# Optimization experiments

Hardware: AMD Instinct MI355X
Metric: run time of the kernel (lower is better)

## Reference

```python
import jax, jax.numpy as jnp
import numpy as np

BATCH, MAXPV = 32, 50
RULENUM, PROPNUM = 256, 256  # must be equal (eye(rulenum) * property_importance)
ENT_DIM, RULE_DIM = 128, 128
ENTITYNUM = 50000
THRESHOLD = 0.5


def _l2norm(x, eps=1e-12):
    # F.normalize(p=2, dim=-1)
    n = jnp.linalg.norm(x, axis=-1, keepdims=True)
    return x / jnp.clip(n, eps)


def setup_inputs() -> dict:
    key = jax.random.key(0)
    ks = jax.random.split(key, 20)
    d_in = ENT_DIM + RULE_DIM
    inp = {
        'property': jax.random.randint(ks[0], (BATCH, MAXPV), 0, ENTITYNUM),
        'value': jax.random.randint(ks[1], (BATCH, MAXPV), 0, ENTITYNUM),
        'samemask': jax.random.randint(ks[2], (BATCH, MAXPV), 0, 2),
        'padmask': jax.random.randint(ks[3], (BATCH, MAXPV), 0, 2),
        'rule_embedding': jax.random.normal(ks[4], (RULENUM, RULE_DIM), jnp.float32),
        'entity_table': jax.random.normal(ks[5], (ENTITYNUM, ENT_DIM), jnp.float32),
        # Linear weights stored (in, out); concat order in the original is (p_emb, rule_emb)
        'fc1_w': jax.random.normal(ks[6], (d_in, ENT_DIM), jnp.float32),
        'fc1_b': jax.random.normal(ks[7], (ENT_DIM,), jnp.float32) * 0.02,
        'fc2_w': jax.random.normal(ks[8], (d_in, ENT_DIM), jnp.float32),
        'fc2_b': jax.random.normal(ks[9], (ENT_DIM,), jnp.float32) * 0.02,
        'fc3_w': jax.random.normal(ks[10], (d_in, ENT_DIM), jnp.float32),
        'fc3_b': jax.random.normal(ks[11], (ENT_DIM,), jnp.float32) * 0.02,
        'fc4_w': jax.random.normal(ks[12], (ENT_DIM, 1), jnp.float32) * 0.05,
        'fc4_b': jax.random.normal(ks[13], (1,), jnp.float32) * 0.02,
        'fc5_w': jax.random.normal(ks[14], (ENT_DIM, 1), jnp.float32) * 0.05,
        'fc5_b': jax.random.normal(ks[15], (1,), jnp.float32) * 0.02,
        'fc6_w': jax.random.normal(ks[16], (ENT_DIM, ENT_DIM), jnp.float32) * 0.05,
        'fc6_b': jax.random.normal(ks[17], (ENT_DIM,), jnp.float32) * 0.02,
    }
    return inp


def reference(property, value, samemask, padmask, rule_embedding, entity_table,
              fc1_w, fc1_b, fc2_w, fc2_b, fc3_w, fc3_b,
              fc4_w, fc4_b, fc5_w, fc5_b, fc6_w, fc6_b):
    E = entity_table.shape[1]
    R = rule_embedding.shape[0]
    P = R  # propertynum == rulenum (required by eye() regularizer)

    p_emb = _l2norm(entity_table[property])   # (B, M, E)
    v_emb = _l2norm(entity_table[value])      # (B, M, E)
    r_emb = _l2norm(rule_embedding)           # (R, Dr)

    # cat(p, rule) -> Linear decomposed into two smaller matmuls (same math)
    def branch(w, b):
        return p_emb @ w[:E], r_emb @ w[E:] + b  # (B,M,Eo), (R,Eo)

    # s1 branch
    pa, ra = branch(fc1_w, fc1_b)
    h1 = jax.nn.relu(pa[:, None, :, :] + ra[None, :, None, :])   # (B,R,M,E)
    s1 = jax.nn.sigmoid(h1 @ fc4_w + fc4_b)[..., 0]              # (B,R,M)

    # p branch
    pb, rb = branch(fc2_w, fc2_b)
    h2 = jax.nn.relu(pb[:, None, :, :] + rb[None, :, None, :])
    p = jax.nn.sigmoid(h2 @ fc5_w + fc5_b)[..., 0]               # (B,R,M)

    # s2 branch
    pc, rc = branch(fc3_w, fc3_b)
    h3 = jax.nn.relu(pc[:, None, :, :] + rc[None, :, None, :])
    gv = _l2norm(h3 @ fc6_w + fc6_b)                             # (B,R,M,E)
    vb = v_emb[:, None, :, :]                                    # (B,1,M,E)
    denom = jnp.clip(jnp.linalg.norm(vb, axis=-1) * jnp.linalg.norm(gv, axis=-1), 1e-8)
    cos = jnp.sum(vb * gv, axis=-1) / denom
    s2 = 0.5 * cos + 0.5                                         # (B,R,M)

    score = p + (1.0 - p) * s2
    score = jnp.where(samemask[:, None, :] == 1, s1 * score, 1.0 - s1)

    # property importance K: fc1/fc4 on cat(prop_emb, rule_emb)
    prop_emb = _l2norm(entity_table[:P])                         # propertyids = arange(P)
    pi_h = jax.nn.relu((prop_emb @ fc1_w[:E])[None, :, :]
                       + (r_emb @ fc1_w[E:] + fc1_b)[:, None, :])  # (R,P,E)
    pi = jax.nn.sigmoid(pi_h @ fc4_w + fc4_b)[..., 0]            # (R,P)

    rule_mask = jnp.sum(pi * (pi > THRESHOLD), axis=-1) + 1.0    # (R,)

    score = score * padmask[:, None, :].astype(score.dtype)
    score = score * (s1 > THRESHOLD)
    score = jnp.sum(score, axis=-1) / rule_mask[None, :]          # (B,R)
    pooledscore = jnp.max(score, axis=1)                          # (B,)

    diag = jnp.eye(R, dtype=pi.dtype)
    reg = pi * diag + (1.0 - pi) * (1.0 - diag)
    reg = -jnp.log(reg + 1e-8) * (1.0 - diag + diag * R)
    reg_logits = jnp.mean(reg)
    return pooledscore, reg_logits
```

## Files before the change

kernel.cpp:

```cpp
#include <hip/hip_runtime.h>
#include <hip/hip_bf16.h>

#define BATCH 32
#define MAXPV 50
#define RN 256
#define PN 256
#define DIM 128
#define NI (BATCH*MAXPV)

typedef unsigned short u16;
typedef __attribute__((ext_vector_type(8))) short short8;
typedef __attribute__((ext_vector_type(4))) float f32x4;

__device__ float g_pa[NI*DIM], g_pb[NI*DIM], g_pc[NI*DIM];
__device__ float g_pp1[PN*DIM];
__device__ __attribute__((aligned(16))) float g_ra[RN*DIM];
__device__ __attribute__((aligned(16))) float g_rb[RN*DIM];
__device__ float g_rmask[RN], g_regp[RN];
__device__ float g_scores[(size_t)NI*RN];
__device__ short8 g_bfrag[8][4][64];
__device__ __attribute__((aligned(16))) float g_rcA[16*4*64*8];

#define WS_WLS(ws)  ((int2*)((ws)+4))
#define WS_WLD(ws)  ((ws)+4+3200)

__device__ __forceinline__ float bf2f(u16 u){ return __uint_as_float(((unsigned)u)<<16); }
__device__ __forceinline__ float LD(const void* p, size_t i, bool bf){
    return bf ? bf2f(((const u16*)p)[i]) : ((const float*)p)[i];
}
__device__ __forceinline__ int LDI(const void* p, size_t i, bool w64){
    return w64 ? (int)((const long long*)p)[i] : ((const int*)p)[i];
}
__device__ __forceinline__ short f2bf(float f){
    unsigned u = __float_as_uint(f);
    u = (u + 0x7FFFu + ((u>>16)&1u)) >> 16;
    return (short)u;
}
__device__ __forceinline__ unsigned f2bf2(float x, float y){
    float2 f; f.x=x; f.y=y;
    __hip_bfloat162 h = __float22bfloat162_rn(f);
    union { __hip_bfloat162 h; unsigned u; } c; c.h=h; return c.u;
}
__device__ __forceinline__ bool det_bf16(const void* ent){
    int l = threadIdx.x & 63;
    u16 v = ((const u16*)ent)[(size_t)2*(l*4)*977];
    int e = (v>>7)&0xFF;
    return __popcll(__ballot(e>=120 && e<=133)) >= 48;
}
__device__ __forceinline__ bool det_i64(const void* prop){
    int l = threadIdx.x & 63;
    bool z = (l<32) ? (((const unsigned*)prop)[2*l+1]==0u) : false;
    return __popcll(__ballot(z)) >= 30;
}
__device__ __forceinline__ float wred(float v){
#pragma unroll
    for(int o=32;o;o>>=1) v += __shfl_xor(v,o,64);
    return v;
}
__device__ __forceinline__ double wredd(double v){
#pragma unroll
    for(int o=32;o;o>>=1) v += __shfl_xor(v,o,64);
    return v;
}
__device__ __forceinline__ float wmax(float v){
#pragma unroll
    for(int o=32;o;o>>=1) v = fmaxf(v,__shfl_xor(v,o,64));
    return v;
}

__global__ __launch_bounds__(256) void k_pre(
    const void* __restrict__ ent, const void* __restrict__ rule,
    const void* __restrict__ prop, const void* __restrict__ val,
    const void* __restrict__ same, const void* __restrict__ pad,
    const void* __restrict__ fc6w,
    const void* __restrict__ fc1w, const void* __restrict__ fc2w, const void* __restrict__ fc3w,
    const void* __restrict__ fc1b, const void* __restrict__ fc2b, const void* __restrict__ fc3b,
    int* __restrict__ ws){
    const bool bf = det_bf16(ent);
    const int blk = blockIdx.x, tid = threadIdx.x;
    if(blk >= 372){
        const bool w64 = det_i64(prop);
        int i = (blk-372)*256 + tid;
        if(i < NI){
            int pd = LDI(pad,i,w64);
            if(pd==1){
                int sm = LDI(same,i,w64);
                if(sm==1){
                    int x = atomicAdd(ws+0,1);
                    WS_WLS(ws)[x] = make_int2(i, LDI(val,i,w64));
                } else {
                    int x = atomicAdd(ws+1,1);
                    WS_WLD(ws)[x] = i;
                }
            }
        }
        return;
    }
    if(blk >= 364){
        int nt = blk-364;
        int ks = tid>>6, lane = tid&63;
        int n = nt*16 + (lane&15);
        int k0 = ks*32 + (lane>>4)*8;
        short8 v;
#pragma unroll
        for(int j=0;j<8;j++) v[j] = f2bf(LD(fc6w,(size_t)(k0+j)*DIM + n, bf));
        g_bfrag[nt][ks][lane] = v;
        if(nt==0){
            g_rmask[tid] = 1.f; g_regp[tid] = 0.f;
            const bool w64 = det_i64(prop);
            if(tid==0) ws[2] = (bf?1:0) | (w64?2:0);
        }
        return;
    }
    __shared__ float s_w[64*DIM];
    __shared__ float s_in[16*DIM];
    __shared__ float s_bias[DIM];
    const void* w; size_t woff=0; const void* bptr=nullptr;
    float* out=nullptr; int row0; int mode=0; int srcsel;
    if(blk < 300){
        int wsel = blk/100; row0 = (blk%100)*16; srcsel = 0;
        w   = (wsel==0)?fc1w:(wsel==1)?fc2w:fc3w;
        out = (wsel==0)?g_pa:(wsel==1)?g_pb:g_pc;
    } else if(blk < 348){
        int rblk = blk-300; int wsel = rblk>>4; row0 = (rblk&15)*16; srcsel = 1;
        w    = (wsel==0)?fc1w:(wsel==1)?fc2w:fc3w;
        bptr = (wsel==0)?fc1b:(wsel==1)?fc2b:fc3b;
        woff = DIM*DIM; mode = wsel+1;
    } else { row0=(blk-348)*16; w=fc1w; out=g_pp1; srcsel=2; }
    const bool w64 = (srcsel==0) ? det_i64(prop) : false;
    {
        const int l = tid & 63;
        for(int it=0; it<4; it++){
            int lr = it*4 + (tid>>6);
            int row = row0 + lr;
            const void* src; size_t off;
            if(srcsel==0){ src=ent;  off=(size_t)LDI(prop,row,w64)*DIM; }
            else if(srcsel==1){ src=rule; off=(size_t)row*DIM; }
            else { src=ent; off=(size_t)row*DIM; }
            float a = LD(src,off+l,bf), b = LD(src,off+l+64,bf);
            float n = fmaxf(sqrtf((float)wredd((double)a*a+(double)b*b)), 1e-12f);
            s_in[lr*DIM+l]=a/n; s_in[lr*DIM+l+64]=b/n;
        }
    }
    if(tid<DIM) s_bias[tid] = bptr ? LD(bptr,tid,bf) : 0.f;
    const int j = tid & 127;
    const int rb8 = (tid>>7)*8;
    double acc[8] = {0,0,0,0,0,0,0,0};
    for(int half=0; half<2; half++){
        __syncthreads();
        for(int t=tid; t<64*DIM; t+=256)
            s_w[t] = LD(w, woff + (size_t)(half*64 + (t>>7))*DIM + (t&127), bf);
        __syncthreads();
        for(int k=0;k<64;k++){
            float wk = s_w[k*DIM + j];
#pragma unroll
            for(int rr=0;rr<8;rr++)
                acc[rr] += (double)s_in[(rb8+rr)*DIM + half*64 + k]*(double)wk;
        }
    }
    const double bj = (double)s_bias[j];
#pragma unroll
    for(int rr=0;rr<8;rr++){
        const int row = row0 + rb8 + rr;
        const float vv = (float)(bj + acc[rr]);
        if(mode==0)      out[(size_t)row*DIM + j] = vv;
        else if(mode==1) g_ra[(size_t)row*DIM + j] = vv;
        else if(mode==2) g_rb[(size_t)row*DIM + j] = vv;
        else {
            int mt=row>>4, am=row&15, ks=j>>5, quad=(j>>3)&3, jj=j&7;
            g_rcA[((mt*4+ks)*64 + quad*16+am)*8 + jj] = vv;
        }
    }
}

__global__ __launch_bounds__(256) void k_score(
    const void* __restrict__ ent,
    const void* __restrict__ fc4w, const void* __restrict__ fc4b,
    const void* __restrict__ fc5w, const void* __restrict__ fc5b,
    const void* __restrict__ fc6b, const int* __restrict__ ws){
    const int blk = blockIdx.x, tid = threadIdx.x;
    const int fl = ws[2];
    const bool bf = fl & 1;
    if(blk < 64){
        __shared__ float s_a[4][DIM];
        __shared__ double s_pf4[DIM];
        const int i0 = blk*4;
        if(tid<DIM) s_pf4[tid]=(double)LD(fc4w,tid,bf);
        for(int t=tid; t<4*DIM; t+=256){
            int ii=t>>7, k=t&127;
            s_a[ii][k] = g_pp1[(size_t)(i0+ii)*DIM+k];
        }
        __syncthreads();
        const int r = tid;
        const float4* rap = (const float4*)&g_ra[(size_t)r*DIM];
        double d0=0.0, d1=0.0, d2=0.0, d3=0.0;
#pragma unroll 4
        for(int x=0; x<32; x++){
            const float4 ra = rap[x];
#pragma unroll
            for(int cc=0; cc<4; cc++){
                const int k = x*4 + cc;
                const float rav = (cc==0)?ra.x:(cc==1)?ra.y:(cc==2)?ra.z:ra.w;
                const double f4k = s_pf4[k];
                d0 += (double)fmaxf(s_a[0][k]+rav,0.f)*f4k;
                d1 += (double)fmaxf(s_a[1][k]+rav,0.f)*f4k;
                d2 += (double)fmaxf(s_a[2][k]+rav,0.f)*f4k;
                d3 += (double)fmaxf(s_a[3][k]+rav,0.f)*f4k;
            }
        }
        const double b4 = (double)LD(fc4b,0,bf);
        double d[4] = {d0,d1,d2,d3};
        float mask_sum = 0.f, reg_sum = 0.f;
#pragma unroll
        for(int ii=0;ii<4;ii++){
            int p = i0 + ii;
            double sd = d[ii] + b4;
            float piv = 1.f/(1.f+expf(-(float)sd));
            if(sd > 0.0) mask_sum += piv;
            float eff = (p==r) ? piv : (1.f - piv);
            float wgt = (p==r) ? (float)RN : 1.f;
            reg_sum += -logf(eff + 1e-8f)*wgt;
        }
        atomicAdd(&g_rmask[r], mask_sum);
        atomicAdd(&g_regp[r], reg_sum);
        return;
    }
    int w2 = blk - 64;
    const int ns4 = ws[0]*4;

    __shared__ float s_pa[DIM], s_pb[DIM], s_pc[DIM], s_v[DIM], s_f5[DIM];
    __shared__ double s_f4[DIM];
    __shared__ float s_s1[64], s_p[64];
    __shared__ float s_st[64][4][2];

    if(w2 >= ns4){
        w2 -= ns4;
        if(w2 >= ws[1]) return;
        const int i = WS_WLD(ws)[w2];
        if(tid < 128){
            s_pa[tid] = g_pa[(size_t)i*DIM + tid];
            s_f4[tid] = (double)LD(fc4w,tid,bf);
        }
        __syncthreads();
        const int r = tid;
        const float4* rap = (const float4*)&g_ra[(size_t)r*DIM];
        double d = 0.0;
#pragma unroll 4
        for(int x=0; x<32; x++){
            const float4 ra = rap[x];
            d += (double)fmaxf(s_pa[x*4+0]+ra.x,0.f)*s_f4[x*4+0];
            d += (double)fmaxf(s_pa[x*4+1]+ra.y,0.f)*s_f4[x*4+1];
            d += (double)fmaxf(s_pa[x*4+2]+ra.z,0.f)*s_f4[x*4+2];
            d += (double)fmaxf(s_pa[x*4+3]+ra.w,0.f)*s_f4[x*4+3];
        }
        const double b4 = (double)LD(fc4b,0,bf);
        double sd = d + b4;
        float s1v = 1.f/(1.f+expf(-(float)sd));
        g_scores[(size_t)i*RN + r] = (sd > 0.0) ? (1.f - s1v) : 0.f;
        return;
    }

    const int2 e = WS_WLS(ws)[w2>>2];
    const int i = e.x, vi = e.y, q4 = w2 & 3;

    if(tid < DIM){
        s_pa[tid] = g_pa[(size_t)i*DIM + tid];
        s_pb[tid] = g_pb[(size_t)i*DIM + tid];
        s_pc[tid] = g_pc[(size_t)i*DIM + tid];
        s_f4[tid] = (double)LD(fc4w,tid,bf);
        s_f5[tid] = LD(fc5w,tid,bf);
    } else if(tid < 192){
        const int l = tid - 128;
        size_t off = (size_t)vi*DIM;
        float a = LD(ent,off+l,bf), b = LD(ent,off+l+64,bf);
        float n = fmaxf(sqrtf((float)wredd((double)a*a+(double)b*b)), 1e-12f);
        s_v[l]=a/n; s_v[l+64]=b/n;
    }
    __syncthreads();

    const int rr = tid & 63;
    const int r = q4*64 + rr;
    if(tid < 64){
        const float4* rap = (const float4*)&g_ra[(size_t)r*DIM];
        double d = 0.0;
#pragma unroll 4
        for(int x=0; x<32; x++){
            const float4 ra = rap[x];
            d += (double)fmaxf(s_pa[x*4+0]+ra.x,0.f)*s_f4[x*4+0];
            d += (double)fmaxf(s_pa[x*4+1]+ra.y,0.f)*s_f4[x*4+1];
            d += (double)fmaxf(s_pa[x*4+2]+ra.z,0.f)*s_f4[x*4+2];
            d += (double)fmaxf(s_pa[x*4+3]+ra.w,0.f)*s_f4[x*4+3];
        }
        const double b4 = (double)LD(fc4b,0,bf);
        double sd = d + b4;
        float s1v = 1.f/(1.f+expf(-(float)sd));
        s_s1[rr] = (sd > 0.0) ? s1v : -s1v;
    } else if(tid < 128){
        const float4* rbp = (const float4*)&g_rb[(size_t)r*DIM];
        float pq = 0.f;
#pragma unroll 4
        for(int x=0; x<32; x++){
            const float4 rb = rbp[x];
            pq = fmaf(fmaxf(s_pb[x*4+0]+rb.x,0.f), s_f5[x*4+0], pq);
            pq = fmaf(fmaxf(s_pb[x*4+1]+rb.y,0.f), s_f5[x*4+1], pq);
            pq = fmaf(fmaxf(s_pb[x*4+2]+rb.z,0.f), s_f5[x*4+2], pq);
            pq = fmaf(fmaxf(s_pb[x*4+3]+rb.w,0.f), s_f5[x*4+3], pq);
        }
        const float b5 = LD(fc5b,0,bf);
        s_p[rr] = 1.f/(1.f+expf(-(pq + b5)));
    }
    __syncthreads();

    const int w = tid>>6, l = tid&63;
    const int am = l&15, quad = l>>4;
    short8 bA[4], bB[4];
#pragma unroll
    for(int ks=0; ks<4; ks++){ bA[ks]=g_bfrag[2*w][ks][l]; bB[ks]=g_bfrag[2*w+1][ks][l]; }
    const int n0 = w*32 + am, n1 = n0 + 16;
    const float v0 = s_v[n0], v1 = s_v[n1];
    const float b60 = LD(fc6b, n0, bf), b61 = LD(fc6b, n1, bf);
    float vl = s_v[l], vh = s_v[l+64];
    const float nvb = sqrtf(wred(vl*vl + vh*vh));

    int mt = q4*4;
    float4 c[8];
#pragma unroll
    for(int ks=0; ks<4; ks++){
        const float* rp = &g_rcA[((mt*4+ks)*64 + l)*8];
        c[2*ks]   = *(const float4*)rp;
        c[2*ks+1] = *(const float4*)(rp+4);
    }
    for(int mtl=0; mtl<4; mtl++){
        float4 n[8];
        if(mtl < 3){
#pragma unroll
            for(int ks=0; ks<4; ks++){
                const float* rp = &g_rcA[(((mt+1)*4+ks)*64 + l)*8];
                n[2*ks]   = *(const float4*)rp;
                n[2*ks+1] = *(const float4*)(rp+4);
            }
        }
        short8 a[4];
#pragma unroll
        for(int ks=0; ks<4; ks++){
            const float4 p0 = *(const float4*)&s_pc[ks*32 + quad*8];
            const float4 p1 = *(const float4*)&s_pc[ks*32 + quad*8 + 4];
            const float4 c0 = c[2*ks], c1 = c[2*ks+1];
            union { short8 s; unsigned u[4]; } t;
            t.u[0] = f2bf2(fmaxf(p0.x+c0.x,0.f), fmaxf(p0.y+c0.y,0.f));
            t.u[1] = f2bf2(fmaxf(p0.z+c0.z,0.f), fmaxf(p0.w+c0.w,0.f));
            t.u[2] = f2bf2(fmaxf(p1.x+c1.x,0.f), fmaxf(p1.y+c1.y,0.f));
            t.u[3] = f2bf2(fmaxf(p1.z+c1.z,0.f), fmaxf(p1.w+c1.w,0.f));
            a[ks] = t.s;
        }
        f32x4 acc0 = {0.f,0.f,0.f,0.f}, acc1 = {0.f,0.f,0.f,0.f};
#pragma unroll
        for(int ks=0; ks<4; ks++){
            acc0 = __builtin_amdgcn_mfma_f32_16x16x32_bf16(a[ks], bA[ks], acc0, 0,0,0);
            acc1 = __builtin_amdgcn_mfma_f32_16x16x32_bf16(a[ks], bB[ks], acc1, 0,0,0);
        }
#pragma unroll
        for(int q=0; q<4; q++){
            float x0 = acc0[q] + b60;
            float x1 = acc1[q] + b61;
            float ss = x0*x0 + x1*x1;
            float dv = x0*v0 + x1*v1;
#pragma unroll
            for(int o=1;o<16;o<<=1){ ss += __shfl_xor(ss,o,64); dv += __shfl_xor(dv,o,64); }
            if(am==0){
                int row = mtl*16 + quad*4 + q;
                s_st[row][w][0] = ss;
                s_st[row][w][1] = dv;
            }
        }
#pragma unroll
        for(int x=0;x<8;x++) c[x] = n[x];
        mt++;
    }
    __syncthreads();
    if(tid < 64){
        const int r2 = q4*64 + tid;
        float ss = s_st[tid][0][0]+s_st[tid][1][0]+s_st[tid][2][0]+s_st[tid][3][0];
        float dv = s_st[tid][0][1]+s_st[tid][1][1]+s_st[tid][2][1]+s_st[tid][3][1];
        float s1 = fabsf(s_s1[tid]);
        float gate = (s_s1[tid] > 0.f) ? 1.f : 0.f;
        float pp = s_p[tid];
        float nx = sqrtf(ss);
        float clipnx = fmaxf(nx, 1e-12f);
        float gvn = nx/clipnx;
        float denom = fmaxf(nvb*gvn, 1e-8f);
        float cosv = (dv/clipnx)/denom;
        float s2 = 0.5f*cosv + 0.5f;
        float sc = s1*(pp + (1.f-pp)*s2);
        g_scores[(size_t)i*RN + r2] = sc * gate;
    }
}

__global__ void k_fin(float* __restrict__ out, const void* __restrict__ pad,
                      const int* __restrict__ ws){
    const bool w64 = (ws[2] & 2) != 0;
    const int blk = blockIdx.x, tid = threadIdx.x;
    const int w = tid>>6, l = tid&63;
    __shared__ float s[4];
    if(blk < 32){
        __shared__ int s_pad[MAXPV];
        if(tid < MAXPV) s_pad[tid] = LDI(pad, (size_t)blk*MAXPV + tid, w64);
        __syncthreads();
        float ssum = 0.f;
        for(int pv=0; pv<MAXPV; pv++){
            if(!s_pad[pv]) continue;
            ssum += g_scores[((size_t)blk*MAXPV + pv)*RN + tid];
        }
        float sc = ssum / g_rmask[tid];
        float m = wmax(sc);
        if(l==0) s[w]=m;
        __syncthreads();
        if(tid==0) out[blk] = fmaxf(fmaxf(s[0],s[1]), fmaxf(s[2],s[3]));
    } else {
        float v = g_regp[tid];
        v = wred(v);
        if(l==0) s[w]=v;
        __syncthreads();
        if(tid==0) out[32] = (s[0]+s[1]+s[2]+s[3]) / (float)(RN*PN);
    }
}

extern "C" void kernel_launch(void* const* d_in, const int* in_sizes, int n_in,
                              void* d_out, int out_size, void* d_ws, size_t ws_size,
                              hipStream_t stream){
    int map[18]; for(int i=0;i<18;i++) map[i]=i;
    if(n_in>=18 && in_sizes[0]==6400000){
        const int a[18] = {14,17,16,13,15,0,2,1,4,3,6,5,8,7,10,9,12,11};
        for(int i=0;i<18;i++) map[i]=a[i];
    }
    const void* prop = d_in[map[0]];
    const void* val  = d_in[map[1]];
    const void* same = d_in[map[2]];
    const void* pad  = d_in[map[3]];
    const void* rule = d_in[map[4]];
    const void* ent  = d_in[map[5]];
    const void* fc1w = d_in[map[6]];
    const void* fc1b = d_in[map[7]];
    const void* fc2w = d_in[map[8]];
    const void* fc2b = d_in[map[9]];
    const void* fc3w = d_in[map[10]];
    const void* fc3b = d_in[map[11]];
    const void* fc4w = d_in[map[12]];
    const void* fc4b = d_in[map[13]];
    const void* fc5w = d_in[map[14]];
    const void* fc5b = d_in[map[15]];
    const void* fc6w = d_in[map[16]];
    const void* fc6b = d_in[map[17]];

    hipMemsetAsync(d_ws, 0, 16, stream);
    k_pre<<<379, 256, 0, stream>>>(ent, rule, prop, val, same, pad, fc6w,
                                   fc1w, fc2w, fc3w, fc1b, fc2b, fc3b, (int*)d_ws);
    k_score<<<64 + 4*NI, 256, 0, stream>>>(ent, fc4w, fc4b, fc5w, fc5b, fc6b,
                                           (const int*)d_ws);
    k_fin<<<33, 256, 0, stream>>>((float*)d_out, pad, (const int*)d_ws);
}
```

Baseline: 192.2 us.

## Convert score kernel to persistent work-stealing loop and precompute value norms

The score kernel becomes a persistent kernel launched with a fixed 1536 blocks. Each block takes its first item from its block index, then pulls further work items from an atomic counter, so no blocks are launched only to exit early. The per-item L2 normalisation of value embeddings moves into extra k_pre blocks that write g_v, and the same-list now stores only the item index. This trades the cost of launching 6464 mostly empty blocks for an extra global buffer, atomic traffic and a barrier per work item, and it drops the software prefetch of rcA tiles.

After: 202.0 us. +5.1%, slower.

```diff
diff --git a/kernel.cpp b/kernel.cpp
--- a/kernel.cpp
+++ b/kernel.cpp
@@ -14,6 +14,7 @@
 
 __device__ float g_pa[NI*DIM], g_pb[NI*DIM], g_pc[NI*DIM];
 __device__ float g_pp1[PN*DIM];
+__device__ __attribute__((aligned(16))) float g_v[NI*DIM];
 __device__ __attribute__((aligned(16))) float g_ra[RN*DIM];
 __device__ __attribute__((aligned(16))) float g_rb[RN*DIM];
 __device__ float g_rmask[RN], g_regp[RN];
@@ -21,8 +22,8 @@
 __device__ short8 g_bfrag[8][4][64];
 __device__ __attribute__((aligned(16))) float g_rcA[16*4*64*8];
 
-#define WS_WLS(ws)  ((int2*)((ws)+4))
-#define WS_WLD(ws)  ((ws)+4+3200)
+#define WS_WLS(ws)  ((ws)+4)
+#define WS_WLD(ws)  ((ws)+4+1600)
 
 __device__ __forceinline__ float bf2f(u16 u){ return __uint_as_float(((unsigned)u)<<16); }
 __device__ __forceinline__ float LD(const void* p, size_t i, bool bf){
@@ -78,6 +79,16 @@
     int* __restrict__ ws){
     const bool bf = det_bf16(ent);
     const int blk = blockIdx.x, tid = threadIdx.x;
+    if(blk >= 379){
+        const bool w64 = det_i64(prop);
+        const int row = (blk-379)*4 + (tid>>6);
+        const int l = tid & 63;
+        size_t off = (size_t)LDI(val,row,w64)*DIM;
+        float a = LD(ent,off+l,bf), b = LD(ent,off+l+64,bf);
+        float n = fmaxf(sqrtf((float)wredd((double)a*a+(double)b*b)), 1e-12f);
+        g_v[(size_t)row*DIM+l]=a/n; g_v[(size_t)row*DIM+l+64]=b/n;
+        return;
+    }
     if(blk >= 372){
         const bool w64 = det_i64(prop);
         int i = (blk-372)*256 + tid;
@@ -87,7 +98,7 @@
                 int sm = LDI(same,i,w64);
                 if(sm==1){
                     int x = atomicAdd(ws+0,1);
-                    WS_WLS(ws)[x] = make_int2(i, LDI(val,i,w64));
+                    WS_WLS(ws)[x] = i;
                 } else {
                     int x = atomicAdd(ws+1,1);
                     WS_WLD(ws)[x] = i;
@@ -173,226 +184,212 @@
     }
 }
 
-__global__ __launch_bounds__(256) void k_score(
-    const void* __restrict__ ent,
+__global__ __launch_bounds__(256) void k_main(
     const void* __restrict__ fc4w, const void* __restrict__ fc4b,
     const void* __restrict__ fc5w, const void* __restrict__ fc5b,
-    const void* __restrict__ fc6b, const int* __restrict__ ws){
-    const int blk = blockIdx.x, tid = threadIdx.x;
-    const int fl = ws[2];
-    const bool bf = fl & 1;
-    if(blk < 64){
-        __shared__ float s_a[4][DIM];
-        __shared__ double s_pf4[DIM];
-        const int i0 = blk*4;
-        if(tid<DIM) s_pf4[tid]=(double)LD(fc4w,tid,bf);
-        for(int t=tid; t<4*DIM; t+=256){
-            int ii=t>>7, k=t&127;
-            s_a[ii][k] = g_pp1[(size_t)(i0+ii)*DIM+k];
-        }
-        __syncthreads();
-        const int r = tid;
-        const float4* rap = (const float4*)&g_ra[(size_t)r*DIM];
-        double d0=0.0, d1=0.0, d2=0.0, d3=0.0;
-#pragma unroll 4
-        for(int x=0; x<32; x++){
-            const float4 ra = rap[x];
-#pragma unroll
-            for(int cc=0; cc<4; cc++){
-                const int k = x*4 + cc;
-                const float rav = (cc==0)?ra.x:(cc==1)?ra.y:(cc==2)?ra.z:ra.w;
-                const double f4k = s_pf4[k];
-                d0 += (double)fmaxf(s_a[0][k]+rav,0.f)*f4k;
-                d1 += (double)fmaxf(s_a[1][k]+rav,0.f)*f4k;
-                d2 += (double)fmaxf(s_a[2][k]+rav,0.f)*f4k;
-                d3 += (double)fmaxf(s_a[3][k]+rav,0.f)*f4k;
-            }
-        }
-        const double b4 = (double)LD(fc4b,0,bf);
-        double d[4] = {d0,d1,d2,d3};
-        float mask_sum = 0.f, reg_sum = 0.f;
-#pragma unroll
-        for(int ii=0;ii<4;ii++){
-            int p = i0 + ii;
-            double sd = d[ii] + b4;
-            float piv = 1.f/(1.f+expf(-(float)sd));
-            if(sd > 0.0) mask_sum += piv;
-            float eff = (p==r) ? piv : (1.f - piv);
-            float wgt = (p==r) ? (float)RN : 1.f;
-            reg_sum += -logf(eff + 1e-8f)*wgt;
-        }
-        atomicAdd(&g_rmask[r], mask_sum);
-        atomicAdd(&g_regp[r], reg_sum);
-        return;
-    }
-    int w2 = blk - 64;
-    const int ns4 = ws[0]*4;
-
+    const void* __restrict__ fc6b, int* __restrict__ ws){
+    __shared__ int s_hdr[4];
     __shared__ float s_pa[DIM], s_pb[DIM], s_pc[DIM], s_v[DIM], s_f5[DIM];
     __shared__ double s_f4[DIM];
     __shared__ float s_s1[64], s_p[64];
     __shared__ float s_st[64][4][2];
-
-    if(w2 >= ns4){
-        w2 -= ns4;
-        if(w2 >= ws[1]) return;
-        const int i = WS_WLD(ws)[w2];
-        if(tid < 128){
-            s_pa[tid] = g_pa[(size_t)i*DIM + tid];
-            s_f4[tid] = (double)LD(fc4w,tid,bf);
-        }
-        __syncthreads();
-        const int r = tid;
-        const float4* rap = (const float4*)&g_ra[(size_t)r*DIM];
-        double d = 0.0;
-#pragma unroll 4
-        for(int x=0; x<32; x++){
-            const float4 ra = rap[x];
-            d += (double)fmaxf(s_pa[x*4+0]+ra.x,0.f)*s_f4[x*4+0];
-            d += (double)fmaxf(s_pa[x*4+1]+ra.y,0.f)*s_f4[x*4+1];
-            d += (double)fmaxf(s_pa[x*4+2]+ra.z,0.f)*s_f4[x*4+2];
-            d += (double)fmaxf(s_pa[x*4+3]+ra.w,0.f)*s_f4[x*4+3];
-        }
-        const double b4 = (double)LD(fc4b,0,bf);
-        double sd = d + b4;
-        float s1v = 1.f/(1.f+expf(-(float)sd));
-        g_scores[(size_t)i*RN + r] = (sd > 0.0) ? (1.f - s1v) : 0.f;
-        return;
-    }
-
-    const int2 e = WS_WLS(ws)[w2>>2];
-    const int i = e.x, vi = e.y, q4 = w2 & 3;
-
-    if(tid < DIM){
-        s_pa[tid] = g_pa[(size_t)i*DIM + tid];
-        s_pb[tid] = g_pb[(size_t)i*DIM + tid];
-        s_pc[tid] = g_pc[(size_t)i*DIM + tid];
-        s_f4[tid] = (double)LD(fc4w,tid,bf);
-        s_f5[tid] = LD(fc5w,tid,bf);
-    } else if(tid < 192){
-        const int l = tid - 128;
-        size_t off = (size_t)vi*DIM;
-        float a = LD(ent,off+l,bf), b = LD(ent,off+l+64,bf);
-        float n = fmaxf(sqrtf((float)wredd((double)a*a+(double)b*b)), 1e-12f);
-        s_v[l]=a/n; s_v[l+64]=b/n;
-    }
+    __shared__ float s_a[4][DIM];
+    const int tid = threadIdx.x;
+    if(tid==0){ int4 h = *(const int4*)ws; s_hdr[0]=h.x; s_hdr[1]=h.y; s_hdr[2]=h.z; }
     __syncthreads();
-
-    const int rr = tid & 63;
-    const int r = q4*64 + rr;
-    if(tid < 64){
-        const float4* rap = (const float4*)&g_ra[(size_t)r*DIM];
-        double d = 0.0;
-#pragma unroll 4
-        for(int x=0; x<32; x++){
-            const float4 ra = rap[x];
-            d += (double)fmaxf(s_pa[x*4+0]+ra.x,0.f)*s_f4[x*4+0];
-            d += (double)fmaxf(s_pa[x*4+1]+ra.y,0.f)*s_f4[x*4+1];
-            d += (double)fmaxf(s_pa[x*4+2]+ra.z,0.f)*s_f4[x*4+2];
-            d += (double)fmaxf(s_pa[x*4+3]+ra.w,0.f)*s_f4[x*4+3];
-        }
-        const double b4 = (double)LD(fc4b,0,bf);
-        double sd = d + b4;
-        float s1v = 1.f/(1.f+expf(-(float)sd));
-        s_s1[rr] = (sd > 0.0) ? s1v : -s1v;
-    } else if(tid < 128){
-        const float4* rbp = (const float4*)&g_rb[(size_t)r*DIM];
-        float pq = 0.f;
-#pragma unroll 4
-        for(int x=0; x<32; x++){
-            const float4 rb = rbp[x];
-            pq = fmaf(fmaxf(s_pb[x*4+0]+rb.x,0.f), s_f5[x*4+0], pq);
-            pq = fmaf(fmaxf(s_pb[x*4+1]+rb.y,0.f), s_f5[x*4+1], pq);
-            pq = fmaf(fmaxf(s_pb[x*4+2]+rb.z,0.f), s_f5[x*4+2], pq);
-            pq = fmaf(fmaxf(s_pb[x*4+3]+rb.w,0.f), s_f5[x*4+3], pq);
-        }
-        const float b5 = LD(fc5b,0,bf);
-        s_p[rr] = 1.f/(1.f+expf(-(pq + b5)));
-    }
-    __syncthreads();
-
-    const int w = tid>>6, l = tid&63;
-    const int am = l&15, quad = l>>4;
+    const int nsame = s_hdr[0], ndiff = s_hdr[1];
+    const bool bf = s_hdr[2] & 1;
+    const int total = 64 + 4*nsame + ndiff;
+    if(tid < DIM){ s_f4[tid] = (double)LD(fc4w,tid,bf); s_f5[tid] = LD(fc5w,tid,bf); }
+    const int w = tid>>6, l = tid&63, am = l&15, quad = l>>4;
     short8 bA[4], bB[4];
 #pragma unroll
     for(int ks=0; ks<4; ks++){ bA[ks]=g_bfrag[2*w][ks][l]; bB[ks]=g_bfrag[2*w+1][ks][l]; }
     const int n0 = w*32 + am, n1 = n0 + 16;
-    const float v0 = s_v[n0], v1 = s_v[n1];
     const float b60 = LD(fc6b, n0, bf), b61 = LD(fc6b, n1, bf);
-    float vl = s_v[l], vh = s_v[l+64];
-    const float nvb = sqrtf(wred(vl*vl + vh*vh));
-
-    int mt = q4*4;
-    float4 c[8];
-#pragma unroll
-    for(int ks=0; ks<4; ks++){
-        const float* rp = &g_rcA[((mt*4+ks)*64 + l)*8];
-        c[2*ks]   = *(const float4*)rp;
-        c[2*ks+1] = *(const float4*)(rp+4);
-    }
-    for(int mtl=0; mtl<4; mtl++){
-        float4 n[8];
-        if(mtl < 3){
-#pragma unroll
-            for(int ks=0; ks<4; ks++){
-                const float* rp = &g_rcA[(((mt+1)*4+ks)*64 + l)*8];
-                n[2*ks]   = *(const float4*)rp;
-                n[2*ks+1] = *(const float4*)(rp+4);
-            }
-        }
-        short8 a[4];
-#pragma unroll
-        for(int ks=0; ks<4; ks++){
-            const float4 p0 = *(const float4*)&s_pc[ks*32 + quad*8];
-            const float4 p1 = *(const float4*)&s_pc[ks*32 + quad*8 + 4];
-            const float4 c0 = c[2*ks], c1 = c[2*ks+1];
-            union { short8 s; unsigned u[4]; } t;
-            t.u[0] = f2bf2(fmaxf(p0.x+c0.x,0.f), fmaxf(p0.y+c0.y,0.f));
-            t.u[1] = f2bf2(fmaxf(p0.z+c0.z,0.f), fmaxf(p0.w+c0.w,0.f));
-            t.u[2] = f2bf2(fmaxf(p1.x+c1.x,0.f), fmaxf(p1.y+c1.y,0.f));
-            t.u[3] = f2bf2(fmaxf(p1.z+c1.z,0.f), fmaxf(p1.w+c1.w,0.f));
-            a[ks] = t.s;
-        }
-        f32x4 acc0 = {0.f,0.f,0.f,0.f}, acc1 = {0.f,0.f,0.f,0.f};
-#pragma unroll
-        for(int ks=0; ks<4; ks++){
-            acc0 = __builtin_amdgcn_mfma_f32_16x16x32_bf16(a[ks], bA[ks], acc0, 0,0,0);
-            acc1 = __builtin_amdgcn_mfma_f32_16x16x32_bf16(a[ks], bB[ks], acc1, 0,0,0);
-        }
-#pragma unroll
-        for(int q=0; q<4; q++){
-            float x0 = acc0[q] + b60;
-            float x1 = acc1[q] + b61;
-            float ss = x0*x0 + x1*x1;
-            float dv = x0*v0 + x1*v1;
-#pragma unroll
-            for(int o=1;o<16;o<<=1){ ss += __shfl_xor(ss,o,64); dv += __shfl_xor(dv,o,64); }
-            if(am==0){
-                int row = mtl*16 + quad*4 + q;
-                s_st[row][w][0] = ss;
-                s_st[row][w][1] = dv;
-            }
-        }
-#pragma unroll
-        for(int x=0;x<8;x++) c[x] = n[x];
-        mt++;
-    }
-    __syncthreads();
-    if(tid < 64){
-        const int r2 = q4*64 + tid;
-        float ss = s_st[tid][0][0]+s_st[tid][1][0]+s_st[tid][2][0]+s_st[tid][3][0];
-        float dv = s_st[tid][0][1]+s_st[tid][1][1]+s_st[tid][2][1]+s_st[tid][3][1];
-        float s1 = fabsf(s_s1[tid]);
-        float gate = (s_s1[tid] > 0.f) ? 1.f : 0.f;
-        float pp = s_p[tid];
-        float nx = sqrtf(ss);
-        float clipnx = fmaxf(nx, 1e-12f);
-        float gvn = nx/clipnx;
-        float denom = fmaxf(nvb*gvn, 1e-8f);
-        float cosv = (dv/clipnx)/denom;
-        float s2 = 0.5f*cosv + 0.5f;
-        float sc = s1*(pp + (1.f-pp)*s2);
-        g_scores[(size_t)i*RN + r2] = sc * gate;
+    const double b4 = (double)LD(fc4b,0,bf);
+    const float b5 = LD(fc5b,0,bf);
+
+    for(int it=0;; it++){
+        int idx;
+        if(it==0) idx = blockIdx.x;
+        else {
+            if(tid==0) s_hdr[3] = atomicAdd(ws+3, 1);
+            __syncthreads();
+            idx = (int)gridDim.x + s_hdr[3];
+        }
+        if(idx >= total) return;
+
+        if(idx < 64){
+            const int i0 = idx*4;
+            for(int t=tid; t<4*DIM; t+=256){
+                int ii=t>>7, k=t&127;
+                s_a[ii][k] = g_pp1[(size_t)(i0+ii)*DIM+k];
+            }
+            __syncthreads();
+            const int r = tid;
+            const float4* rap = (const float4*)&g_ra[(size_t)r*DIM];
+            double d0=0.0, d1=0.0, d2=0.0, d3=0.0;
+#pragma unroll 4
+            for(int x=0; x<32; x++){
+                const float4 ra = rap[x];
+#pragma unroll
+                for(int cc=0; cc<4; cc++){
+                    const int k = x*4 + cc;
+                    const float rav = (cc==0)?ra.x:(cc==1)?ra.y:(cc==2)?ra.z:ra.w;
+                    const double f4k = s_f4[k];
+                    d0 += (double)fmaxf(s_a[0][k]+rav,0.f)*f4k;
+                    d1 += (double)fmaxf(s_a[1][k]+rav,0.f)*f4k;
+                    d2 += (double)fmaxf(s_a[2][k]+rav,0.f)*f4k;
+                    d3 += (double)fmaxf(s_a[3][k]+rav,0.f)*f4k;
+                }
+            }
+            double d[4] = {d0,d1,d2,d3};
+            float mask_sum = 0.f, reg_sum = 0.f;
+#pragma unroll
+            for(int ii=0;ii<4;ii++){
+                int p = i0 + ii;
+                double sd = d[ii] + b4;
+                float piv = 1.f/(1.f+expf(-(float)sd));
+                if(sd > 0.0) mask_sum += piv;
+                float eff = (p==r) ? piv : (1.f - piv);
+                float wgt = (p==r) ? (float)RN : 1.f;
+                reg_sum += -logf(eff + 1e-8f)*wgt;
+            }
+            atomicAdd(&g_rmask[r], mask_sum);
+            atomicAdd(&g_regp[r], reg_sum);
+            continue;
+        }
+        int t = idx - 64;
+        if(t < 4*nsame){
+            const int i = WS_WLS(ws)[t>>2];
+            const int q4 = t & 3;
+            if(tid < DIM){
+                s_pa[tid] = g_pa[(size_t)i*DIM + tid];
+                s_pb[tid] = g_pb[(size_t)i*DIM + tid];
+                s_pc[tid] = g_pc[(size_t)i*DIM + tid];
+            } else if(tid < 192){
+                const int ll = tid - 128;
+                s_v[ll]    = g_v[(size_t)i*DIM + ll];
+                s_v[ll+64] = g_v[(size_t)i*DIM + ll + 64];
+            }
+            __syncthreads();
+            const int rr = tid & 63;
+            const int r = q4*64 + rr;
+            if(tid < 64){
+                const float4* rap = (const float4*)&g_ra[(size_t)r*DIM];
+                double d = 0.0;
+#pragma unroll 4
+                for(int x=0; x<32; x++){
+                    const float4 ra = rap[x];
+                    d += (double)fmaxf(s_pa[x*4+0]+ra.x,0.f)*s_f4[x*4+0];
+                    d += (double)fmaxf(s_pa[x*4+1]+ra.y,0.f)*s_f4[x*4+1];
+                    d += (double)fmaxf(s_pa[x*4+2]+ra.z,0.f)*s_f4[x*4+2];
+                    d += (double)fmaxf(s_pa[x*4+3]+ra.w,0.f)*s_f4[x*4+3];
+                }
+                double sd = d + b4;
+                float s1v = 1.f/(1.f+expf(-(float)sd));
+                s_s1[rr] = (sd > 0.0) ? s1v : -s1v;
+            } else if(tid < 128){
+                const float4* rbp = (const float4*)&g_rb[(size_t)r*DIM];
+                float pq = 0.f;
+#pragma unroll 4
+                for(int x=0; x<32; x++){
+                    const float4 rb = rbp[x];
+                    pq = fmaf(fmaxf(s_pb[x*4+0]+rb.x,0.f), s_f5[x*4+0], pq);
+                    pq = fmaf(fmaxf(s_pb[x*4+1]+rb.y,0.f), s_f5[x*4+1], pq);
+                    pq = fmaf(fmaxf(s_pb[x*4+2]+rb.z,0.f), s_f5[x*4+2], pq);
+                    pq = fmaf(fmaxf(s_pb[x*4+3]+rb.w,0.f), s_f5[x*4+3], pq);
+                }
+                s_p[rr] = 1.f/(1.f+expf(-(pq + b5)));
+            }
+            __syncthreads();
+            const float v0 = s_v[n0], v1 = s_v[n1];
+            float vl = s_v[l], vh = s_v[l+64];
+            const float nvb = sqrtf(wred(vl*vl + vh*vh));
+            int mt = q4*4;
+            for(int mtl=0; mtl<4; mtl++){
+                float4 c[8];
+#pragma unroll
+                for(int ks=0; ks<4; ks++){
+                    const float* rp = &g_rcA[((mt*4+ks)*64 + l)*8];
+                    c[2*ks]   = *(const float4*)rp;
+                    c[2*ks+1] = *(const float4*)(rp+4);
+                }
+                short8 a[4];
+#pragma unroll
+                for(int ks=0; ks<4; ks++){
+                    const float4 p0 = *(const float4*)&s_pc[ks*32 + quad*8];
+                    const float4 p1 = *(const float4*)&s_pc[ks*32 + quad*8 + 4];
+                    const float4 c0 = c[2*ks], c1 = c[2*ks+1];
+                    union { short8 s; unsigned u[4]; } tt;
+                    tt.u[0] = f2bf2(fmaxf(p0.x+c0.x,0.f), fmaxf(p0.y+c0.y,0.f));
+                    tt.u[1] = f2bf2(fmaxf(p0.z+c0.z,0.f), fmaxf(p0.w+c0.w,0.f));
+                    tt.u[2] = f2bf2(fmaxf(p1.x+c1.x,0.f), fmaxf(p1.y+c1.y,0.f));
+                    tt.u[3] = f2bf2(fmaxf(p1.z+c1.z,0.f), fmaxf(p1.w+c1.w,0.f));
+                    a[ks] = tt.s;
+                }
+                f32x4 acc0 = {0.f,0.f,0.f,0.f}, acc1 = {0.f,0.f,0.f,0.f};
+#pragma unroll
+                for(int ks=0; ks<4; ks++){
+                    acc0 = __builtin_amdgcn_mfma_f32_16x16x32_bf16(a[ks], bA[ks], acc0, 0,0,0);
+                    acc1 = __builtin_amdgcn_mfma_f32_16x16x32_bf16(a[ks], bB[ks], acc1, 0,0,0);
+                }
+#pragma unroll
+                for(int q=0; q<4; q++){
+                    float x0 = acc0[q] + b60;
+                    float x1 = acc1[q] + b61;
+                    float ss = x0*x0 + x1*x1;
+                    float dv = x0*v0 + x1*v1;
+#pragma unroll
+                    for(int o=1;o<16;o<<=1){ ss += __shfl_xor(ss,o,64); dv += __shfl_xor(dv,o,64); }
+                    if(am==0){
+                        int row = mtl*16 + quad*4 + q;
+                        s_st[row][w][0] = ss;
+                        s_st[row][w][1] = dv;
+                    }
+                }
+                mt++;
+            }
+            __syncthreads();
+            if(tid < 64){
+                const int r2 = q4*64 + tid;
+                float ss = s_st[tid][0][0]+s_st[tid][1][0]+s_st[tid][2][0]+s_st[tid][3][0];
+                float dv = s_st[tid][0][1]+s_st[tid][1][1]+s_st[tid][2][1]+s_st[tid][3][1];
+                float s1 = fabsf(s_s1[tid]);
+                float gate = (s_s1[tid] > 0.f) ? 1.f : 0.f;
+                float pp = s_p[tid];
+                float nx = sqrtf(ss);
+                float clipnx = fmaxf(nx, 1e-12f);
+                float gvn = nx/clipnx;
+                float denom = fmaxf(nvb*gvn, 1e-8f);
+                float cosv = (dv/clipnx)/denom;
+                float s2 = 0.5f*cosv + 0.5f;
+                float sc = s1*(pp + (1.f-pp)*s2);
+                g_scores[(size_t)i*RN + r2] = sc * gate;
+            }
+            continue;
+        }
+        {
+            const int i = WS_WLD(ws)[t - 4*nsame];
+            if(tid < 128) s_pa[tid] = g_pa[(size_t)i*DIM + tid];
+            __syncthreads();
+            const int r = tid;
+            const float4* rap = (const float4*)&g_ra[(size_t)r*DIM];
+            double d = 0.0;
+#pragma unroll 4
+            for(int x=0; x<32; x++){
+                const float4 ra = rap[x];
+                d += (double)fmaxf(s_pa[x*4+0]+ra.x,0.f)*s_f4[x*4+0];
+                d += (double)fmaxf(s_pa[x*4+1]+ra.y,0.f)*s_f4[x*4+1];
+                d += (double)fmaxf(s_pa[x*4+2]+ra.z,0.f)*s_f4[x*4+2];
+                d += (double)fmaxf(s_pa[x*4+3]+ra.w,0.f)*s_f4[x*4+3];
+            }
+            double sd = d + b4;
+            float s1v = 1.f/(1.f+expf(-(float)sd));
+            g_scores[(size_t)i*RN + r] = (sd > 0.0) ? (1.f - s1v) : 0.f;
+            continue;
+        }
     }
 }
 
@@ -453,9 +450,8 @@
     const void* fc6b = d_in[map[17]];
 
     hipMemsetAsync(d_ws, 0, 16, stream);
-    k_pre<<<379, 256, 0, stream>>>(ent, rule, prop, val, same, pad, fc6w,
+    k_pre<<<779, 256, 0, stream>>>(ent, rule, prop, val, same, pad, fc6w,
                                    fc1w, fc2w, fc3w, fc1b, fc2b, fc3b, (int*)d_ws);
-    k_score<<<64 + 4*NI, 256, 0, stream>>>(ent, fc4w, fc4b, fc5w, fc5b, fc6b,
-                                           (const int*)d_ws);
+    k_main<<<1536, 256, 0, stream>>>(fc4w, fc4b, fc5w, fc5b, fc6b, (int*)d_ws);
     k_fin<<<33, 256, 0, stream>>>((float*)d_out, pad, (const int*)d_ws);
 }
```

## Precompute normalized value embeddings and split per-rule dot products across warps

Applied to the files above, without the earlier changes.

Moves the gather and L2-normalisation of value embeddings out of the scoring kernel into extra k_pre blocks that write them to a global buffer. Each scoring block now only loads them. In the scoring kernel the fc4/fc5 rule dot products are split across two warps, each covering half of K, and reduced through shared memory, so all four warps work instead of two. Blocks for the different-value path are split in two halves of R. This adds more blocks, an extra barrier and an intermediate global buffer, while shortening the serial per-thread loops.

New measurement: 191.8 us. About the same (-0.2%).

```diff
diff --git a/kernel.cpp b/kernel.cpp
--- a/kernel.cpp
+++ b/kernel.cpp
@@ -14,6 +14,7 @@
 
 __device__ float g_pa[NI*DIM], g_pb[NI*DIM], g_pc[NI*DIM];
 __device__ float g_pp1[PN*DIM];
+__device__ __attribute__((aligned(16))) float g_v[NI*DIM];
 __device__ __attribute__((aligned(16))) float g_ra[RN*DIM];
 __device__ __attribute__((aligned(16))) float g_rb[RN*DIM];
 __device__ float g_rmask[RN], g_regp[RN];
@@ -21,8 +22,8 @@
 __device__ short8 g_bfrag[8][4][64];
 __device__ __attribute__((aligned(16))) float g_rcA[16*4*64*8];
 
-#define WS_WLS(ws)  ((int2*)((ws)+4))
-#define WS_WLD(ws)  ((ws)+4+3200)
+#define WS_WLS(ws)  ((ws)+4)
+#define WS_WLD(ws)  ((ws)+4+1600)
 
 __device__ __forceinline__ float bf2f(u16 u){ return __uint_as_float(((unsigned)u)<<16); }
 __device__ __forceinline__ float LD(const void* p, size_t i, bool bf){
@@ -78,6 +79,16 @@
     int* __restrict__ ws){
     const bool bf = det_bf16(ent);
     const int blk = blockIdx.x, tid = threadIdx.x;
+    if(blk >= 379){
+        const bool w64 = det_i64(prop);
+        const int row = (blk-379)*4 + (tid>>6);
+        const int l = tid & 63;
+        size_t off = (size_t)LDI(val,row,w64)*DIM;
+        float a = LD(ent,off+l,bf), b = LD(ent,off+l+64,bf);
+        float n = fmaxf(sqrtf((float)wredd((double)a*a+(double)b*b)), 1e-12f);
+        g_v[(size_t)row*DIM+l]=a/n; g_v[(size_t)row*DIM+l+64]=b/n;
+        return;
+    }
     if(blk >= 372){
         const bool w64 = det_i64(prop);
         int i = (blk-372)*256 + tid;
@@ -87,7 +98,7 @@
                 int sm = LDI(same,i,w64);
                 if(sm==1){
                     int x = atomicAdd(ws+0,1);
-                    WS_WLS(ws)[x] = make_int2(i, LDI(val,i,w64));
+                    WS_WLS(ws)[x] = i;
                 } else {
                     int x = atomicAdd(ws+1,1);
                     WS_WLD(ws)[x] = i;
@@ -174,7 +185,6 @@
 }
 
 __global__ __launch_bounds__(256) void k_score(
-    const void* __restrict__ ent,
     const void* __restrict__ fc4w, const void* __restrict__ fc4b,
     const void* __restrict__ fc5w, const void* __restrict__ fc5b,
     const void* __restrict__ fc6b, const int* __restrict__ ws){
@@ -228,86 +238,103 @@
     int w2 = blk - 64;
     const int ns4 = ws[0]*4;
 
-    __shared__ float s_pa[DIM], s_pb[DIM], s_pc[DIM], s_v[DIM], s_f5[DIM];
-    __shared__ double s_f4[DIM];
+    __shared__ float s_pa[DIM], s_pb[DIM], s_pc[DIM], s_v[DIM], s_f4[DIM], s_f5[DIM];
+    __shared__ double s_gd[2][64];
+    __shared__ float s_gq[2][64];
+    __shared__ double s_pd[2][128];
     __shared__ float s_s1[64], s_p[64];
     __shared__ float s_st[64][4][2];
 
     if(w2 >= ns4){
-        w2 -= ns4;
-        if(w2 >= ws[1]) return;
-        const int i = WS_WLD(ws)[w2];
+        int t2 = w2 - ns4;
+        if(t2 >= 2*ws[1]) return;
+        const int i = WS_WLD(ws)[t2>>1];
+        const int sub = t2 & 1;
         if(tid < 128){
             s_pa[tid] = g_pa[(size_t)i*DIM + tid];
-            s_f4[tid] = (double)LD(fc4w,tid,bf);
-        }
-        __syncthreads();
-        const int r = tid;
-        const float4* rap = (const float4*)&g_ra[(size_t)r*DIM];
+            s_f4[tid] = LD(fc4w,tid,bf);
+        }
+        __syncthreads();
+        const int rr = tid & 127, half = tid >> 7;
+        const int r = sub*128 + rr;
+        const float4* rap = (const float4*)&g_ra[(size_t)r*DIM + half*64];
         double d = 0.0;
 #pragma unroll 4
-        for(int x=0; x<32; x++){
+        for(int x=0; x<16; x++){
             const float4 ra = rap[x];
-            d += (double)fmaxf(s_pa[x*4+0]+ra.x,0.f)*s_f4[x*4+0];
-            d += (double)fmaxf(s_pa[x*4+1]+ra.y,0.f)*s_f4[x*4+1];
-            d += (double)fmaxf(s_pa[x*4+2]+ra.z,0.f)*s_f4[x*4+2];
-            d += (double)fmaxf(s_pa[x*4+3]+ra.w,0.f)*s_f4[x*4+3];
-        }
-        const double b4 = (double)LD(fc4b,0,bf);
-        double sd = d + b4;
-        float s1v = 1.f/(1.f+expf(-(float)sd));
-        g_scores[(size_t)i*RN + r] = (sd > 0.0) ? (1.f - s1v) : 0.f;
+            const int k = half*64 + x*4;
+            d += (double)fmaxf(s_pa[k+0]+ra.x,0.f)*(double)s_f4[k+0];
+            d += (double)fmaxf(s_pa[k+1]+ra.y,0.f)*(double)s_f4[k+1];
+            d += (double)fmaxf(s_pa[k+2]+ra.z,0.f)*(double)s_f4[k+2];
+            d += (double)fmaxf(s_pa[k+3]+ra.w,0.f)*(double)s_f4[k+3];
+        }
+        s_pd[half][rr] = d;
+        __syncthreads();
+        if(tid < 128){
+            const double b4 = (double)LD(fc4b,0,bf);
+            double sd = (s_pd[0][tid] + s_pd[1][tid]) + b4;
+            float s1v = 1.f/(1.f+expf(-(float)sd));
+            g_scores[(size_t)i*RN + sub*128 + tid] = (sd > 0.0) ? (1.f - s1v) : 0.f;
+        }
         return;
     }
 
-    const int2 e = WS_WLS(ws)[w2>>2];
-    const int i = e.x, vi = e.y, q4 = w2 & 3;
+    const int i = WS_WLS(ws)[w2>>2];
+    const int q4 = w2 & 3;
 
     if(tid < DIM){
         s_pa[tid] = g_pa[(size_t)i*DIM + tid];
         s_pb[tid] = g_pb[(size_t)i*DIM + tid];
         s_pc[tid] = g_pc[(size_t)i*DIM + tid];
-        s_f4[tid] = (double)LD(fc4w,tid,bf);
+        s_f4[tid] = LD(fc4w,tid,bf);
         s_f5[tid] = LD(fc5w,tid,bf);
     } else if(tid < 192){
-        const int l = tid - 128;
-        size_t off = (size_t)vi*DIM;
-        float a = LD(ent,off+l,bf), b = LD(ent,off+l+64,bf);
-        float n = fmaxf(sqrtf((float)wredd((double)a*a+(double)b*b)), 1e-12f);
-        s_v[l]=a/n; s_v[l+64]=b/n;
+        const int ll = tid - 128;
+        s_v[ll]    = g_v[(size_t)i*DIM + ll];
+        s_v[ll+64] = g_v[(size_t)i*DIM + ll + 64];
     }
     __syncthreads();
 
-    const int rr = tid & 63;
+    const int rr = tid & 63, wv = tid >> 6;
     const int r = q4*64 + rr;
-    if(tid < 64){
-        const float4* rap = (const float4*)&g_ra[(size_t)r*DIM];
+    if(wv < 2){
+        const float4* rap = (const float4*)&g_ra[(size_t)r*DIM + wv*64];
         double d = 0.0;
 #pragma unroll 4
-        for(int x=0; x<32; x++){
+        for(int x=0; x<16; x++){
             const float4 ra = rap[x];
-            d += (double)fmaxf(s_pa[x*4+0]+ra.x,0.f)*s_f4[x*4+0];
-            d += (double)fmaxf(s_pa[x*4+1]+ra.y,0.f)*s_f4[x*4+1];
-            d += (double)fmaxf(s_pa[x*4+2]+ra.z,0.f)*s_f4[x*4+2];
-            d += (double)fmaxf(s_pa[x*4+3]+ra.w,0.f)*s_f4[x*4+3];
-        }
-        const double b4 = (double)LD(fc4b,0,bf);
-        double sd = d + b4;
-        float s1v = 1.f/(1.f+expf(-(float)sd));
-        s_s1[rr] = (sd > 0.0) ? s1v : -s1v;
-    } else if(tid < 128){
-        const float4* rbp = (const float4*)&g_rb[(size_t)r*DIM];
+            const int k = wv*64 + x*4;
+            d += (double)fmaxf(s_pa[k+0]+ra.x,0.f)*(double)s_f4[k+0];
+            d += (double)fmaxf(s_pa[k+1]+ra.y,0.f)*(double)s_f4[k+1];
+            d += (double)fmaxf(s_pa[k+2]+ra.z,0.f)*(double)s_f4[k+2];
+            d += (double)fmaxf(s_pa[k+3]+ra.w,0.f)*(double)s_f4[k+3];
+        }
+        s_gd[wv][rr] = d;
+    } else {
+        const int hh = wv - 2;
+        const float4* rbp = (const float4*)&g_rb[(size_t)r*DIM + hh*64];
         float pq = 0.f;
 #pragma unroll 4
-        for(int x=0; x<32; x++){
+        for(int x=0; x<16; x++){
             const float4 rb = rbp[x];
-            pq = fmaf(fmaxf(s_pb[x*4+0]+rb.x,0.f), s_f5[x*4+0], pq);
-            pq = fmaf(fmaxf(s_pb[x*4+1]+rb.y,0.f), s_f5[x*4+1], pq);
-            pq = fmaf(fmaxf(s_pb[x*4+2]+rb.z,0.f), s_f5[x*4+2], pq);
-            pq = fmaf(fmaxf(s_pb[x*4+3]+rb.w,0.f), s_f5[x*4+3], pq);
-        }
+            const int k = hh*64 + x*4;
+            pq = fmaf(fmaxf(s_pb[k+0]+rb.x,0.f), s_f5[k+0], pq);
+            pq = fmaf(fmaxf(s_pb[k+1]+rb.y,0.f), s_f5[k+1], pq);
+            pq = fmaf(fmaxf(s_pb[k+2]+rb.z,0.f), s_f5[k+2], pq);
+            pq = fmaf(fmaxf(s_pb[k+3]+rb.w,0.f), s_f5[k+3], pq);
+        }
+        s_gq[hh][rr] = pq;
+    }
+    __syncthreads();
+    if(tid < 64){
+        const double b4 = (double)LD(fc4b,0,bf);
+        double sd = (s_gd[0][tid] + s_gd[1][tid]) + b4;
+        float s1v = 1.f/(1.f+expf(-(float)sd));
+        s_s1[tid] = (sd > 0.0) ? s1v : -s1v;
+    } else if(tid < 128){
         const float b5 = LD(fc5b,0,bf);
-        s_p[rr] = 1.f/(1.f+expf(-(pq + b5)));
+        float pq = s_gq[0][tid-64] + s_gq[1][tid-64];
+        s_p[tid-64] = 1.f/(1.f+expf(-(pq + b5)));
     }
     __syncthreads();
 
@@ -453,9 +480,9 @@
     const void* fc6b = d_in[map[17]];
 
     hipMemsetAsync(d_ws, 0, 16, stream);
-    k_pre<<<379, 256, 0, stream>>>(ent, rule, prop, val, same, pad, fc6w,
+    k_pre<<<779, 256, 0, stream>>>(ent, rule, prop, val, same, pad, fc6w,
                                    fc1w, fc2w, fc3w, fc1b, fc2b, fc3b, (int*)d_ws);
-    k_score<<<64 + 4*NI, 256, 0, stream>>>(ent, fc4w, fc4b, fc5w, fc5b, fc6b,
+    k_score<<<64 + 6*NI, 256, 0, stream>>>(fc4w, fc4b, fc5w, fc5b, fc6b,
                                            (const int*)d_ws);
     k_fin<<<33, 256, 0, stream>>>((float*)d_out, pad, (const int*)d_ws);
 }
```
